# Performance work log

Measured on AMD Instinct MI355X. Metric: run time of the kernel, lower is better.

## Reference

```python
import jax, jax.numpy as jnp
import numpy as np

N = 100000      # nodes
E = 1600000     # edges
G = 1024        # graphs in batch
H = 128         # graph_hidden
F_IN = 38
DEPTH = 4
EPS = 1e-5


def setup_inputs() -> dict:
    key = jax.random.key(0)
    ks = jax.random.split(key, 16)
    inp = {
        "h": jax.random.normal(ks[0], (N, F_IN), jnp.float32),
        "src": jax.random.randint(ks[1], (E,), 0, N, jnp.int32),
        "dst": jax.random.randint(ks[2], (E,), 0, N, jnp.int32),
        "node2graph": jnp.sort(jax.random.randint(ks[3], (N,), 0, G, jnp.int32)),
        "W1": jax.random.normal(ks[4], (F_IN, H), jnp.float32) * 0.1,
        "b1": jnp.zeros((H,), jnp.float32),
        "g1": jnp.ones((H,), jnp.float32),
        "be1": jnp.zeros((H,), jnp.float32),
        "W2s": jax.random.normal(ks[5], (DEPTH - 1, H, H), jnp.float32) * 0.1,
        "b2s": jnp.zeros((DEPTH - 1, H), jnp.float32),
        "g2s": jnp.ones((DEPTH - 1, H), jnp.float32),
        "be2s": jnp.zeros((DEPTH - 1, H), jnp.float32),
        "aw": jax.random.normal(ks[6], (H, 1), jnp.float32) * 0.1,
        "ab": jnp.zeros((1,), jnp.float32),
        "Wf1": jax.random.normal(ks[7], (H, 512), jnp.float32) * 0.1,
        "bf1": jnp.zeros((512,), jnp.float32),
        "gf1": jnp.ones((512,), jnp.float32),
        "bef1": jnp.zeros((512,), jnp.float32),
        "Wl": jax.random.normal(ks[8], (512, 256), jnp.float32) * 0.05,
        "bl": jnp.zeros((256,), jnp.float32),
        "gl": jnp.ones((256,), jnp.float32),
        "bel": jnp.zeros((256,), jnp.float32),
        "Wf2": jax.random.normal(ks[9], (256, 67), jnp.float32) * 0.05,
        "bf2": jnp.zeros((67,), jnp.float32),
    }
    return inp


def _bn(x, g, b):
    # BatchNorm1d in training mode: batch stats (biased variance), eps=1e-5.
    m = jnp.mean(x, axis=0)
    v = jnp.mean(jnp.square(x - m), axis=0)
    return g * (x - m) * jax.lax.rsqrt(v + EPS) + b


def reference(h, src, dst, node2graph,
              W1, b1, g1, be1, W2s, b2s, g2s, be2s,
              aw, ab, Wf1, bf1, gf1, bef1, Wl, bl, gl, bel, Wf2, bf2):
    ones_e = jnp.ones((E,), h.dtype)
    deg_out = jax.ops.segment_sum(ones_e, src, num_segments=N)
    deg_in = jax.ops.segment_sum(ones_e, dst, num_segments=N)
    ns = jax.lax.rsqrt(jnp.maximum(deg_out, 1.0))  # src-side D^{-1/2}
    nd = jax.lax.rsqrt(jnp.maximum(deg_in, 1.0))   # dst-side D^{-1/2}

    def gconv(x, W, b):
        # DGL GraphConv norm='both': D_dst^{-1/2} A D_src^{-1/2} x W + b
        msg = (x * ns[:, None])[src]                      # [E, F] gather
        agg = jax.ops.segment_sum(msg, dst, num_segments=N)
        return (agg * nd[:, None]) @ W + b

    # dropout p = 0.0 -> identity
    x = jax.nn.relu(_bn(gconv(h, W1, b1), g1, be1))
    for i in range(DEPTH - 1):
        x = jax.nn.relu(_bn(gconv(x, W2s[i], b2s[i]), g2s[i], be2s[i]))

    # WeightAndSum readout: sigmoid-gated segment sum over nodes per graph
    atom_weights = x @ aw + ab                            # [N, 1] (pre-sigmoid, returned)
    w = jax.nn.sigmoid(atom_weights)
    hg = jax.ops.segment_sum(x * w, node2graph, num_segments=G)  # [G, H]

    y = jax.nn.relu(_bn(hg @ Wf1 + bf1, gf1, bef1))
    y = jax.nn.relu(_bn(y @ Wl + bl, gl, bel))
    y = jax.nn.sigmoid(y @ Wf2 + bf2)                     # [G, 67]
    return (y, atom_weights)
```

## Files before the change

kernel.cpp:

```cpp
#include <hip/hip_runtime.h>
#include <math.h>

#define NN 100000
#define NE 1600000
#define NG 1024
#define MAXDEG 64
#define EPSB 1e-5f

typedef _Float16 h16;
typedef __attribute__((ext_vector_type(2))) _Float16 h16x2;
typedef __attribute__((ext_vector_type(4))) _Float16 h16x4;
typedef __attribute__((ext_vector_type(8))) _Float16 h16x8;
typedef __attribute__((ext_vector_type(4))) float f32x4;

static __device__ __forceinline__ float sigmoidf_(float x){ return 1.f/(1.f+__expf(-x)); }

__global__ void k_fillall(const int* __restrict__ src, const int* __restrict__ dst,
                          int* __restrict__ degO, int* __restrict__ cnt, int* __restrict__ eidx){
  int e = blockIdx.x*256 + threadIdx.x;
  if (e < NE){
    int s = src[e], d = dst[e];
    atomicAdd(&degO[s], 1);
    int p = atomicAdd(&cnt[d], 1);
    if (p < MAXDEG) eidx[d*MAXDEG + p] = s;
  }
}

__global__ void k_prepg(const int* __restrict__ deg2, const int* __restrict__ n2g,
                        int* __restrict__ eidx, float* __restrict__ ns, float* __restrict__ nd,
                        int* __restrict__ gs, int* __restrict__ ge, float* __restrict__ stats,
                        h16* __restrict__ XA, h16* __restrict__ XB){
  int v = blockIdx.x*256 + threadIdx.x;
  if (v < NN){
    int dO = deg2[v], dI = deg2[NN + v];
    ns[v] = rsqrtf(fmaxf((float)dO, 1.f));
    nd[v] = rsqrtf(fmaxf((float)dI, 1.f));
    int deg = dI > MAXDEG ? MAXDEG : dI;
    int ad = (deg + 7) & ~7;
    if (ad < 8) ad = 8;
    if (ad > MAXDEG) ad = MAXDEG;
    for (int i = deg; i < ad; i++) eidx[v*MAXDEG + i] = NN;
    int g = n2g[v];
    if (v == 0) gs[g] = 0;
    else { int gp = n2g[v-1]; if (gp != g){ gs[g] = v; ge[gp] = v; } }
    if (v == NN-1) ge[g] = NN;
  }
  if (v == NN) ns[NN] = 0.f;
  if (blockIdx.x == 0){
    int t = threadIdx.x;
    for (int j = t; j < 4096; j += 256) stats[j] = 0.f;
    if (t < 128){ XA[(size_t)NN*128 + t] = (h16)0.f; XB[(size_t)NN*128 + t] = (h16)0.f; }
  }
}

__global__ void k_convall(const float* __restrict__ W1, const float* __restrict__ W2s,
                          const float* __restrict__ Wf1, const float* __restrict__ Wl,
                          h16* __restrict__ W1t, h16* __restrict__ W2t,
                          h16* __restrict__ Wf1t, h16* __restrict__ Wlt){
  int i = blockIdx.x*256 + threadIdx.x;
  if (i < 8192){
    int c = i >> 6, k = i & 63;
    W1t[i] = (k < 38) ? (h16)W1[(size_t)k*128 + c] : (h16)0.f;
  } else if (i < 57344){
    int j = i - 8192; int l = j >> 14; int r = j & 16383;
    int c = r >> 7, k = r & 127;
    W2t[j] = (h16)W2s[(size_t)l*16384 + (size_t)k*128 + c];
  } else if (i < 122880){
    int j = i - 57344; int c = j >> 7, k = j & 127;
    Wf1t[j] = (h16)Wf1[(size_t)k*512 + c];
  } else if (i < 253952){
    int j = i - 122880; int c = j >> 9, k = j & 511;
    Wlt[j] = (h16)Wl[(size_t)k*256 + c];
  }
}

__global__ void k_prep1(const float* __restrict__ h, const float* __restrict__ ns,
                        h16* __restrict__ hn){
  int i = blockIdx.x*256 + threadIdx.x;
  if (i >= (NN+1)*40) return;
  int v = i / 40, c = i - v*40;
  float val = (v < NN && c < 38) ? h[(size_t)v*38 + c]*ns[v] : 0.f;
  hn[i] = (h16)val;
}

__global__ __launch_bounds__(256)
void k_gs40(const h16* __restrict__ hn, const int* __restrict__ eidx,
            const int* __restrict__ degI, const float* __restrict__ nd,
            h16* __restrict__ A38){
  int v = (blockIdx.x*256 + threadIdx.x) >> 6;
  int lane = threadIdx.x & 63;
  if (v >= NN) return;
  int deg = degI[v]; if (deg > MAXDEG) deg = MAXDEG;
  int deg8 = (deg + 7) & ~7; if (deg8 < 8) deg8 = 8; if (deg8 > MAXDEG) deg8 = MAXDEG;
  const int* row = eidx + v*MAXDEG;
  int g = lane / 20;
  int c0 = 2*(lane % 20);
  bool act = (lane < 40);
  int gg = g & 1;
  float a0 = 0.f, a1 = 0.f;
  int4 s4 = *(const int4*)(row + 4*gg);
  h16x2 u0={}, u1={}, u2={}, u3={};
  if (act){
    u0 = *(const h16x2*)(hn + (size_t)s4.x*40 + c0);
    u1 = *(const h16x2*)(hn + (size_t)s4.y*40 + c0);
    u2 = *(const h16x2*)(hn + (size_t)s4.z*40 + c0);
    u3 = *(const h16x2*)(hn + (size_t)s4.w*40 + c0);
  }
  for (int e = 0; e < deg8; e += 8){
    int nx = (e + 8 < deg8) ? e + 8 : e;
    int4 s4n = *(const int4*)(row + nx + 4*gg);
    h16x2 n0={}, n1={}, n2={}, n3={};
    if (act){
      n0 = *(const h16x2*)(hn + (size_t)s4n.x*40 + c0);
      n1 = *(const h16x2*)(hn + (size_t)s4n.y*40 + c0);
      n2 = *(const h16x2*)(hn + (size_t)s4n.z*40 + c0);
      n3 = *(const h16x2*)(hn + (size_t)s4n.w*40 + c0);
    }
    a0 += ((float)u0[0] + (float)u1[0]) + ((float)u2[0] + (float)u3[0]);
    a1 += ((float)u0[1] + (float)u1[1]) + ((float)u2[1] + (float)u3[1]);
    u0=n0; u1=n1; u2=n2; u3=n3;
  }
  float b0 = __shfl(a0, lane + 20);
  float b1 = __shfl(a1, lane + 20);
  if (lane < 20){
    float ndv = nd[v];
    h16x2 o; o[0] = (h16)((a0 + b0)*ndv); o[1] = (h16)((a1 + b1)*ndv);
    *(h16x2*)(A38 + (size_t)v*64 + c0) = o;
  } else if (lane < 32){
    h16x2 o; o[0] = (h16)0.f; o[1] = (h16)0.f;
    *(h16x2*)(A38 + (size_t)v*64 + 40 + 2*(lane - 20)) = o;
  }
}

__global__ __launch_bounds__(256)
void k_gs128(const h16* __restrict__ X, const int* __restrict__ eidx,
             const int* __restrict__ degI, const float* __restrict__ ns,
             const float* __restrict__ nd, const float* __restrict__ stats,
             const float* __restrict__ gam, const float* __restrict__ bet,
             h16* __restrict__ agg){
  __shared__ float scs[128], shs[128];
  int t = threadIdx.x;
  if (t < 128){
    float m = stats[t]*(1.f/(float)NN);
    float var = fmaxf(stats[128+t]*(1.f/(float)NN) - m*m, 0.f);
    float inv = rsqrtf(var + EPSB);
    float sc = gam[t]*inv;
    scs[t] = sc; shs[t] = fmaf(-sc, m, bet[t]);
  }
  __syncthreads();
  int v = (blockIdx.x*256 + t) >> 6;
  int lane = t & 63;
  if (v >= NN) return;
  int deg = degI[v]; if (deg > MAXDEG) deg = MAXDEG;
  int deg8 = (deg + 7) & ~7; if (deg8 < 8) deg8 = 8; if (deg8 > MAXDEG) deg8 = MAXDEG;
  const int* row = eidx + v*MAXDEG;
  int half = lane >> 5;
  int c0 = 4*(lane & 31);
  float4 sc = *(const float4*)&scs[c0];
  float4 sh = *(const float4*)&shs[c0];
  float a0=0.f, a1=0.f, a2=0.f, a3=0.f;
  int4 s4 = *(const int4*)(row + 4*half);
  float w0=ns[s4.x], w1=ns[s4.y], w2=ns[s4.z], w3=ns[s4.w];
  h16x4 u0 = *(const h16x4*)(X + (size_t)s4.x*128 + c0);
  h16x4 u1 = *(const h16x4*)(X + (size_t)s4.y*128 + c0);
  h16x4 u2 = *(const h16x4*)(X + (size_t)s4.z*128 + c0);
  h16x4 u3 = *(const h16x4*)(X + (size_t)s4.w*128 + c0);
  for (int e = 0; e < deg8; e += 8){
    int nx = (e + 8 < deg8) ? e + 8 : e;
    int4 s4n = *(const int4*)(row + nx + 4*half);
    float v0=ns[s4n.x], v1=ns[s4n.y], v2=ns[s4n.z], v3=ns[s4n.w];
    h16x4 n0 = *(const h16x4*)(X + (size_t)s4n.x*128 + c0);
    h16x4 n1 = *(const h16x4*)(X + (size_t)s4n.y*128 + c0);
    h16x4 n2 = *(const h16x4*)(X + (size_t)s4n.z*128 + c0);
    h16x4 n3 = *(const h16x4*)(X + (size_t)s4n.w*128 + c0);
    a0 = fmaf(fmaxf(fmaf((float)u0[0], sc.x, sh.x), 0.f), w0, a0);
    a1 = fmaf(fmaxf(fmaf((float)u0[1], sc.y, sh.y), 0.f), w0, a1);
    a2 = fmaf(fmaxf(fmaf((float)u0[2], sc.z, sh.z), 0.f), w0, a2);
    a3 = fmaf(fmaxf(fmaf((float)u0[3], sc.w, sh.w), 0.f), w0, a3);
    a0 = fmaf(fmaxf(fmaf((float)u1[0], sc.x, sh.x), 0.f), w1, a0);
    a1 = fmaf(fmaxf(fmaf((float)u1[1], sc.y, sh.y), 0.f), w1, a1);
    a2 = fmaf(fmaxf(fmaf((float)u1[2], sc.z, sh.z), 0.f), w1, a2);
    a3 = fmaf(fmaxf(fmaf((float)u1[3], sc.w, sh.w), 0.f), w1, a3);
    a0 = fmaf(fmaxf(fmaf((float)u2[0], sc.x, sh.x), 0.f), w2, a0);
    a1 = fmaf(fmaxf(fmaf((float)u2[1], sc.y, sh.y), 0.f), w2, a1);
    a2 = fmaf(fmaxf(fmaf((float)u2[2], sc.z, sh.z), 0.f), w2, a2);
    a3 = fmaf(fmaxf(fmaf((float)u2[3], sc.w, sh.w), 0.f), w2, a3);
    a0 = fmaf(fmaxf(fmaf((float)u3[0], sc.x, sh.x), 0.f), w3, a0);
    a1 = fmaf(fmaxf(fmaf((float)u3[1], sc.y, sh.y), 0.f), w3, a1);
    a2 = fmaf(fmaxf(fmaf((float)u3[2], sc.z, sh.z), 0.f), w3, a2);
    a3 = fmaf(fmaxf(fmaf((float)u3[3], sc.w, sh.w), 0.f), w3, a3);
    u0=n0; u1=n1; u2=n2; u3=n3;
    w0=v0; w1=v1; w2=v2; w3=v3;
  }
  a0 += __shfl_xor(a0, 32);
  a1 += __shfl_xor(a1, 32);
  a2 += __shfl_xor(a2, 32);
  a3 += __shfl_xor(a3, 32);
  if (half == 0){
    float ndv = nd[v];
    h16x4 o;
    o[0] = (h16)(a0*ndv); o[1] = (h16)(a1*ndv);
    o[2] = (h16)(a2*ndv); o[3] = (h16)(a3*ndv);
    *(h16x4*)(agg + (size_t)v*128 + c0) = o;
  }
}

__global__ __launch_bounds__(256)
void k_mgemm(const h16* __restrict__ A, const h16* __restrict__ Wt,
             const float* __restrict__ bias, h16* __restrict__ Cout,
             float* __restrict__ stats, int M, int K, int Nc){
  __shared__ h16 As[128][72];
  __shared__ h16 Bs[128][72];
  __shared__ float sred[2][128];
  int m0 = blockIdx.x*128, n0 = blockIdx.y*128;
  int t = threadIdx.x, w = t>>6, lane = t&63;
  int wr = (w>>1)*64, wc = (w&1)*64;
  f32x4 acc[4][4] = {};

  int ar = t>>3;
  int ac = (t&7)*8;
  for (int k0=0; k0<K; k0+=64){
    #pragma unroll
    for (int rr=0; rr<128; rr+=32){
      int gm = m0 + ar + rr;
      h16x8 val = {};
      if (gm < M) val = *(const h16x8*)(A + (size_t)gm*K + k0 + ac);
      *(h16x8*)&As[ar+rr][ac] = val;
    }
    #pragma unroll
    for (int rr=0; rr<128; rr+=32){
      int gc = n0 + ar + rr;
      h16x8 val = {};
      if (gc < Nc) val = *(const h16x8*)(Wt + (size_t)gc*K + k0 + ac);
      *(h16x8*)&Bs[ar+rr][ac] = val;
    }
    __syncthreads();
    int rsel = lane & 15;
    #pragma unroll
    for (int kk=0; kk<64; kk+=32){
      int ksel = kk + (lane>>4)*8;
      h16x8 af[4], bfr[4];
      #pragma unroll
      for (int i=0;i<4;i++) af[i]  = *(const h16x8*)&As[wr + i*16 + rsel][ksel];
      #pragma unroll
      for (int j=0;j<4;j++) bfr[j] = *(const h16x8*)&Bs[wc + j*16 + rsel][ksel];
      #pragma unroll
      for (int i=0;i<4;i++)
        #pragma unroll
        for (int j=0;j<4;j++)
          acc[i][j] = __builtin_amdgcn_mfma_f32_16x16x32_f16(af[i], bfr[j], acc[i][j], 0, 0, 0);
    }
    __syncthreads();
  }

  float csum[4] = {}, csq[4] = {};
  int colsel = lane & 15, rowsel = (lane>>4)*4;
  #pragma unroll
  for (int j=0;j<4;j++){
    int gc = n0 + wc + j*16 + colsel;
    float bv = (gc < Nc) ? bias[gc] : 0.f;
    #pragma unroll
    for (int i=0;i<4;i++){
      #pragma unroll
      for (int r=0;r<4;r++){
        int gm = m0 + wr + i*16 + rowsel + r;
        if (gm < M && gc < Nc){
          float v = acc[i][j][r] + bv;
          Cout[(size_t)gm*Nc + gc] = (h16)v;
          csum[j] += v; csq[j] += v*v;
        }
      }
    }
  }
  if (stats){
    ((float*)sred)[t] = 0.f;
    __syncthreads();
    #pragma unroll
    for (int j=0;j<4;j++){
      int lc = wc + j*16 + colsel;
      atomicAdd(&sred[0][lc], csum[j]);
      atomicAdd(&sred[1][lc], csq[j]);
    }
    __syncthreads();
    if (t < 128){
      int gc = n0 + t;
      if (gc < Nc){
        atomicAdd(&stats[gc],      sred[0][t]);
        atomicAdd(&stats[Nc + gc], sred[1][t]);
      }
    }
  }
}

__global__ __launch_bounds__(256)
void k_readout(const h16* __restrict__ X, const float* __restrict__ stats,
               const float* __restrict__ gam, const float* __restrict__ bet,
               const float* __restrict__ aw, const float* __restrict__ ab,
               const int* __restrict__ gs, const int* __restrict__ ge,
               float* __restrict__ awout, h16* __restrict__ hg){
  __shared__ float scs[128], shs[128], awv[128];
  __shared__ float red[4][128];
  int t = threadIdx.x;
  if (t < 128){
    float m = stats[t]*(1.f/(float)NN);
    float var = fmaxf(stats[128+t]*(1.f/(float)NN) - m*m, 0.f);
    float inv = rsqrtf(var + EPSB);
    float sc = gam[t]*inv;
    scs[t] = sc; shs[t] = fmaf(-sc, m, bet[t]);
    awv[t] = aw[t];
  }
  __syncthreads();
  int g = blockIdx.x;
  int s = gs[g], e = ge[g];
  int w = t>>6, lane = t&63, c0 = 2*lane;
  float sc0=scs[c0], sc1=scs[c0+1], sh0=shs[c0], sh1=shs[c0+1];
  float aw0=awv[c0], aw1=awv[c0+1];
  float ab0 = ab[0];
  float acc0=0.f, acc1=0.f;
  for (int n = s + w; n < e; n += 4){
    h16x2 u = *(const h16x2*)(X + (size_t)n*128 + c0);
    float x0 = fmaxf(fmaf((float)u[0], sc0, sh0), 0.f);
    float x1 = fmaxf(fmaf((float)u[1], sc1, sh1), 0.f);
    float d = x0*aw0 + x1*aw1;
    #pragma unroll
    for (int o=32;o>0;o>>=1) d += __shfl_xor(d, o);
    float tv = d + ab0;
    if (lane == 0) awout[n] = tv;
    float wn = sigmoidf_(tv);
    acc0 = fmaf(x0, wn, acc0);
    acc1 = fmaf(x1, wn, acc1);
  }
  red[w][c0] = acc0; red[w][c0+1] = acc1;
  __syncthreads();
  if (w == 0){
    float a0 = red[0][c0] + red[1][c0] + red[2][c0] + red[3][c0];
    float a1 = red[0][c0+1] + red[1][c0+1] + red[2][c0+1] + red[3][c0+1];
    h16x2 o; o[0] = (h16)a0; o[1] = (h16)a1;
    *(h16x2*)(hg + (size_t)g*128 + c0) = o;
  }
}

__global__ __launch_bounds__(256)
void k_bnapply_f(const h16* __restrict__ X, h16* __restrict__ Y,
                 const float* __restrict__ stats, const float* __restrict__ gam,
                 const float* __restrict__ bet, float invM, int C, int totalPairs){
  __shared__ float scs[512], shs[512];
  int t = threadIdx.x;
  for (int c = t; c < C; c += 256){
    float m = stats[c]*invM;
    float var = fmaxf(stats[C+c]*invM - m*m, 0.f);
    float inv = rsqrtf(var + EPSB);
    float sc = gam[c]*inv;
    scs[c] = sc; shs[c] = fmaf(-sc, m, bet[c]);
  }
  __syncthreads();
  int i = blockIdx.x*256 + t;
  if (i >= totalPairs) return;
  int pm = (C >> 1) - 1;
  int c0 = 2*(i & pm);
  h16x2 u = *(const h16x2*)(X + 2*(size_t)i);
  float x0 = fmaxf(fmaf((float)u[0], scs[c0],   shs[c0]),   0.f);
  float x1 = fmaxf(fmaf((float)u[1], scs[c0+1], shs[c0+1]), 0.f);
  h16x2 o; o[0] = (h16)x0; o[1] = (h16)x1;
  *(h16x2*)(Y + 2*(size_t)i) = o;
}

__global__ void k_final(const h16* __restrict__ y2, const float* __restrict__ Wf2,
                        const float* __restrict__ bf2v, float* __restrict__ out){
  int idx = blockIdx.x*256 + threadIdx.x;
  if (idx >= NG*67) return;
  int g = idx / 67, c = idx % 67;
  float s = bf2v[c];
  const h16* row = y2 + (size_t)g*256;
  for (int k=0;k<256;k+=2){
    h16x2 u = *(const h16x2*)(row + k);
    s = fmaf((float)u[0], Wf2[(size_t)k*67 + c], s);
    s = fmaf((float)u[1], Wf2[(size_t)(k+1)*67 + c], s);
  }
  out[(size_t)g*67 + c] = sigmoidf_(s);
}

extern "C" void kernel_launch(void* const* d_in, const int* in_sizes, int n_in,
                              void* d_out, int out_size, void* d_ws, size_t ws_size,
                              hipStream_t stream){
  const float* h   = (const float*)d_in[0];
  const int*   src = (const int*)d_in[1];
  const int*   dst = (const int*)d_in[2];
  const int*   n2g = (const int*)d_in[3];
  const float* W1  = (const float*)d_in[4];
  const float* b1  = (const float*)d_in[5];
  const float* g1  = (const float*)d_in[6];
  const float* be1 = (const float*)d_in[7];
  const float* W2s = (const float*)d_in[8];
  const float* b2s = (const float*)d_in[9];
  const float* g2s = (const float*)d_in[10];
  const float* be2s= (const float*)d_in[11];
  const float* aw  = (const float*)d_in[12];
  const float* ab  = (const float*)d_in[13];
  const float* Wf1 = (const float*)d_in[14];
  const float* bf1 = (const float*)d_in[15];
  const float* gf1 = (const float*)d_in[16];
  const float* bef1= (const float*)d_in[17];
  const float* Wl  = (const float*)d_in[18];
  const float* bl  = (const float*)d_in[19];
  const float* gl  = (const float*)d_in[20];
  const float* bel = (const float*)d_in[21];
  const float* Wf2 = (const float*)d_in[22];
  const float* bf2v= (const float*)d_in[23];
  float* out = (float*)d_out;

  char* p = (char*)d_ws;
  auto carve = [&](size_t bytes)->void*{
    void* r = (void*)p; p += (bytes + 255) & ~(size_t)255; return r;
  };
  int* deg2 = (int*)carve((size_t)2*NN*4);
  int* gsge = (int*)carve((size_t)2*NG*4);
  h16* XA   = (h16*)carve((size_t)(NN+1)*128*2);
  h16* XB   = (h16*)carve((size_t)(NN+1)*128*2);
  h16* hn   = (h16*)carve((size_t)(NN+1)*40*2);
  h16* A38  = (h16*)carve((size_t)NN*64*2);
  int* eidx = (int*)carve((size_t)NN*MAXDEG*4);
  float* ns = (float*)carve((size_t)(NN+1)*4);
  float* nd = (float*)carve((size_t)NN*4);
  h16* hg   = (h16*)carve((size_t)NG*128*2);
  h16* y1p  = (h16*)carve((size_t)NG*512*2);
  h16* y1   = (h16*)carve((size_t)NG*512*2);
  h16* y2p  = (h16*)carve((size_t)NG*256*2);
  h16* y2   = (h16*)carve((size_t)NG*256*2);
  float* stats = (float*)carve(4096*4);
  h16* W1t  = (h16*)carve((size_t)128*64*2);
  h16* W2t  = (h16*)carve((size_t)3*128*128*2);
  h16* Wf1t = (h16*)carve((size_t)512*128*2);
  h16* Wlt  = (h16*)carve((size_t)256*512*2);

  int* gs = gsge;
  int* ge = gsge + NG;
  float* st1  = stats;
  float* st2a = stats + 256;
  float* st2b = stats + 512;
  float* st2c = stats + 768;
  float* stf1 = stats + 1024;
  float* stl  = stats + 2048;
  float* st2[3] = { st2a, st2b, st2c };

  hipMemsetAsync(deg2, 0, (size_t)2*NN*4 + (size_t)2*NG*4, stream);

  k_convall<<<(253952+255)/256, 256, 0, stream>>>(W1, W2s, Wf1, Wl, W1t, W2t, Wf1t, Wlt);
  k_fillall<<<(NE+255)/256, 256, 0, stream>>>(src, dst, deg2, deg2 + NN, eidx);
  k_prepg  <<<(NN+1+255)/256, 256, 0, stream>>>(deg2, n2g, eidx, ns, nd, gs, ge, stats, XA, XB);

  const int* degI = deg2 + NN;
  const int nodeBlocks = (NN + 3)/4;
  const int gemmBlocks = (NN + 127)/128;

  k_prep1<<<((NN+1)*40+255)/256, 256, 0, stream>>>(h, ns, hn);
  k_gs40 <<<nodeBlocks, 256, 0, stream>>>(hn, eidx, degI, nd, A38);
  k_mgemm<<<dim3(gemmBlocks,1), 256, 0, stream>>>(A38, W1t, b1, XA, st1, NN, 64, 128);

  const float* stPrev[3] = { st1, st2a, st2b };
  const float* gPrev[3]  = { g1, g2s, g2s + 128 };
  const float* bePrev[3] = { be1, be2s, be2s + 128 };
  for (int i=0;i<3;i++){
    k_gs128<<<nodeBlocks, 256, 0, stream>>>(XA, eidx, degI, ns, nd,
                                            stPrev[i], gPrev[i], bePrev[i], XB);
    k_mgemm<<<dim3(gemmBlocks,1), 256, 0, stream>>>(XB, W2t + (size_t)i*128*128, b2s + i*128,
                                                    XA, st2[i], NN, 128, 128);
  }

  k_readout<<<NG, 256, 0, stream>>>(XA, st2c, g2s + 256, be2s + 256, aw, ab,
                                    gs, ge, out + (size_t)NG*67, hg);

  k_mgemm<<<dim3(NG/128, 4), 256, 0, stream>>>(hg, Wf1t, bf1, y1p, stf1, NG, 128, 512);
  k_bnapply_f<<<(NG*256+255)/256, 256, 0, stream>>>(y1p, y1, stf1, gf1, bef1,
                                                    1.0f/(float)NG, 512, NG*256);
  k_mgemm<<<dim3(NG/128, 2), 256, 0, stream>>>(y1, Wlt, bl, y2p, stl, NG, 512, 256);
  k_bnapply_f<<<(NG*128+255)/256, 256, 0, stream>>>(y2p, y2, stl, gl, bel,
                                                    1.0f/(float)NG, 256, NG*128);
  k_final<<<(NG*67+255)/256, 256, 0, stream>>>(y2, Wf2, bf2v, out);
}
```

Baseline: 725.1 us.

## Replace global-atomic adjacency build with bucketed counting sort via shared-memory histograms

Degree counting and neighbour-list filling no longer use per-edge global atomics. Edges are now bucketed by dst/64 and src/64 with a per-block shared-memory histogram, a three-pass prefix scan and a scatter. Per-bucket blocks then build eidx, the degrees and the normalisers using shared-memory atomics. The aim is to cut contention and scattered global atomic traffic, at the cost of six extra launches and an extra 12.8MB sorted buffer pass. The graph start/end computation also now fills empty graphs, which replaces the memset.

```diff
diff --git a/kernel.cpp b/kernel.cpp
--- a/kernel.cpp
+++ b/kernel.cpp
@@ -7,6 +7,12 @@
 #define MAXDEG 64
 #define EPSB 1e-5f
 
+#define NBUK 1563
+#define NBLK 256
+#define EPB  6250
+#define FLAT (2*NBUK*NBLK)
+#define NCH  ((FLAT + 1023)/1024)
+
 typedef _Float16 h16;
 typedef __attribute__((ext_vector_type(2))) _Float16 h16x2;
 typedef __attribute__((ext_vector_type(4))) _Float16 h16x4;
@@ -15,35 +21,148 @@
 
 static __device__ __forceinline__ float sigmoidf_(float x){ return 1.f/(1.f+__expf(-x)); }
 
-__global__ void k_fillall(const int* __restrict__ src, const int* __restrict__ dst,
-                          int* __restrict__ degO, int* __restrict__ cnt, int* __restrict__ eidx){
-  int e = blockIdx.x*256 + threadIdx.x;
-  if (e < NE){
-    int s = src[e], d = dst[e];
-    atomicAdd(&degO[s], 1);
-    int p = atomicAdd(&cnt[d], 1);
-    if (p < MAXDEG) eidx[d*MAXDEG + p] = s;
-  }
-}
-
-__global__ void k_prepg(const int* __restrict__ deg2, const int* __restrict__ n2g,
-                        int* __restrict__ eidx, float* __restrict__ ns, float* __restrict__ nd,
+__global__ __launch_bounds__(256)
+void k_hist(const int* __restrict__ src, const int* __restrict__ dst,
+            int* __restrict__ blockHist){
+  __shared__ int hd[NBUK];
+  __shared__ int hs[NBUK];
+  int b = blockIdx.x, t = threadIdx.x;
+  for (int j = t; j < NBUK; j += 256){ hd[j] = 0; hs[j] = 0; }
+  __syncthreads();
+  int e0 = b*EPB, e1 = e0 + EPB;
+  for (int i = e0 + t; i < e1; i += 256){
+    atomicAdd(&hd[dst[i]>>6], 1);
+    atomicAdd(&hs[src[i]>>6], 1);
+  }
+  __syncthreads();
+  for (int j = t; j < NBUK; j += 256){
+    blockHist[(size_t)j*NBLK + b] = hd[j];
+    blockHist[(size_t)(NBUK + j)*NBLK + b] = hs[j];
+  }
+}
+
+__global__ __launch_bounds__(256)
+void k_scan1(int* __restrict__ data, int* __restrict__ csum){
+  __shared__ int s[256];
+  int blk = blockIdx.x, t = threadIdx.x;
+  int base = blk*1024 + t*4;
+  int v0=0,v1=0,v2=0,v3=0;
+  if (base+0 < FLAT) v0 = data[base+0];
+  if (base+1 < FLAT) v1 = data[base+1];
+  if (base+2 < FLAT) v2 = data[base+2];
+  if (base+3 < FLAT) v3 = data[base+3];
+  int tot = v0+v1+v2+v3;
+  s[t] = tot; __syncthreads();
+  for (int o=1;o<256;o<<=1){ int x = (t>=o)? s[t-o]:0; __syncthreads(); s[t]+=x; __syncthreads(); }
+  int excl = s[t] - tot;
+  if (t == 255) csum[blk] = s[255];
+  if (base+0 < FLAT) data[base+0] = excl;
+  if (base+1 < FLAT) data[base+1] = excl + v0;
+  if (base+2 < FLAT) data[base+2] = excl + v0 + v1;
+  if (base+3 < FLAT) data[base+3] = excl + v0 + v1 + v2;
+}
+
+__global__ void k_scan2(int* __restrict__ csum){
+  __shared__ int s[1024];
+  int t = threadIdx.x;
+  int x = (t < NCH) ? csum[t] : 0;
+  s[t] = x; __syncthreads();
+  for (int o=1;o<1024;o<<=1){ int y = (t>=o)? s[t-o]:0; __syncthreads(); s[t]+=y; __syncthreads(); }
+  if (t < NCH) csum[t] = s[t] - x;
+}
+
+__global__ __launch_bounds__(256)
+void k_scan3(int* __restrict__ data, const int* __restrict__ csum){
+  int blk = blockIdx.x, t = threadIdx.x;
+  int add = csum[blk];
+  int base = blk*1024 + t*4;
+  if (base+0 < FLAT) data[base+0] += add;
+  if (base+1 < FLAT) data[base+1] += add;
+  if (base+2 < FLAT) data[base+2] += add;
+  if (base+3 < FLAT) data[base+3] += add;
+}
+
+__global__ __launch_bounds__(256)
+void k_scatter(const int* __restrict__ src, const int* __restrict__ dst,
+               const int* __restrict__ scanned, unsigned int* __restrict__ sortedBuf){
+  __shared__ int bd[NBUK];
+  __shared__ int bs[NBUK];
+  int b = blockIdx.x, t = threadIdx.x;
+  for (int j = t; j < NBUK; j += 256){
+    bd[j] = scanned[(size_t)j*NBLK + b];
+    bs[j] = scanned[(size_t)(NBUK + j)*NBLK + b];
+  }
+  __syncthreads();
+  int e0 = b*EPB, e1 = e0 + EPB;
+  for (int i = e0 + t; i < e1; i += 256){
+    int s = src[i], d = dst[i];
+    int posD = atomicAdd(&bd[d>>6], 1);
+    sortedBuf[posD] = (unsigned int)s | ((unsigned int)(d & 63) << 20);
+    int posS = atomicAdd(&bs[s>>6], 1);
+    sortedBuf[posS] = (unsigned int)s;
+  }
+}
+
+__global__ __launch_bounds__(256)
+void k_build(const unsigned int* __restrict__ sortedBuf, const int* __restrict__ scanned,
+             int* __restrict__ eidx, int* __restrict__ degI,
+             float* __restrict__ ns, float* __restrict__ nd){
+  __shared__ int cnt[64];
+  int k = blockIdx.x, t = threadIdx.x;
+  int v0 = k*64;
+  int nv = NN - v0; if (nv > 64) nv = 64;
+  if (t < 64) cnt[t] = 0;
+  __syncthreads();
+  int startD = scanned[(size_t)k*NBLK];
+  int endD   = scanned[(size_t)(k+1)*NBLK];
+  for (int i = startD + t; i < endD; i += 256){
+    unsigned int u = sortedBuf[i];
+    int lid = (int)(u >> 20);
+    int slot = atomicAdd(&cnt[lid], 1);
+    if (slot < MAXDEG) eidx[(size_t)(v0 + lid)*MAXDEG + slot] = (int)(u & 0xFFFFFu);
+  }
+  __syncthreads();
+  if (t < nv){
+    int v = v0 + t;
+    int dI = cnt[t];
+    degI[v] = dI;
+    nd[v] = rsqrtf(fmaxf((float)dI, 1.f));
+    int c = dI > MAXDEG ? MAXDEG : dI;
+    int ad = (c + 7) & ~7; if (ad < 8) ad = 8; if (ad > MAXDEG) ad = MAXDEG;
+    for (int i = c; i < ad; i++) eidx[(size_t)v*MAXDEG + i] = NN;
+  }
+  __syncthreads();
+  if (t < 64) cnt[t] = 0;
+  __syncthreads();
+  int startS = scanned[(size_t)(NBUK + k)*NBLK];
+  int endS   = (k+1 < NBUK) ? scanned[(size_t)(NBUK + k + 1)*NBLK] : 2*NE;
+  for (int i = startS + t; i < endS; i += 256){
+    atomicAdd(&cnt[sortedBuf[i] & 63u], 1);
+  }
+  __syncthreads();
+  if (t < nv) ns[v0 + t] = rsqrtf(fmaxf((float)cnt[t], 1.f));
+}
+
+__global__ void k_prepg(const int* __restrict__ n2g,
                         int* __restrict__ gs, int* __restrict__ ge, float* __restrict__ stats,
-                        h16* __restrict__ XA, h16* __restrict__ XB){
+                        float* __restrict__ ns, h16* __restrict__ XA, h16* __restrict__ XB){
   int v = blockIdx.x*256 + threadIdx.x;
   if (v < NN){
-    int dO = deg2[v], dI = deg2[NN + v];
-    ns[v] = rsqrtf(fmaxf((float)dO, 1.f));
-    nd[v] = rsqrtf(fmaxf((float)dI, 1.f));
-    int deg = dI > MAXDEG ? MAXDEG : dI;
-    int ad = (deg + 7) & ~7;
-    if (ad < 8) ad = 8;
-    if (ad > MAXDEG) ad = MAXDEG;
-    for (int i = deg; i < ad; i++) eidx[v*MAXDEG + i] = NN;
     int g = n2g[v];
-    if (v == 0) gs[g] = 0;
-    else { int gp = n2g[v-1]; if (gp != g){ gs[g] = v; ge[gp] = v; } }
-    if (v == NN-1) ge[g] = NN;
+    if (v == 0){
+      for (int q = 0; q <= g; q++) gs[q] = 0;
+      for (int q = 0; q < g; q++) ge[q] = 0;
+    } else {
+      int gp = n2g[v-1];
+      if (gp != g){
+        for (int q = gp+1; q <= g; q++) gs[q] = v;
+        for (int q = gp; q < g; q++) ge[q] = v;
+      }
+    }
+    if (v == NN-1){
+      for (int q = g+1; q < NG; q++) gs[q] = NN;
+      for (int q = g; q < NG; q++) ge[q] = NN;
+    }
   }
   if (v == NN) ns[NN] = 0.f;
   if (blockIdx.x == 0){
@@ -413,15 +532,18 @@
   auto carve = [&](size_t bytes)->void*{
     void* r = (void*)p; p += (bytes + 255) & ~(size_t)255; return r;
   };
-  int* deg2 = (int*)carve((size_t)2*NN*4);
-  int* gsge = (int*)carve((size_t)2*NG*4);
   h16* XA   = (h16*)carve((size_t)(NN+1)*128*2);
   h16* XB   = (h16*)carve((size_t)(NN+1)*128*2);
   h16* hn   = (h16*)carve((size_t)(NN+1)*40*2);
   h16* A38  = (h16*)carve((size_t)NN*64*2);
   int* eidx = (int*)carve((size_t)NN*MAXDEG*4);
+  unsigned int* sortedBuf = (unsigned int*)carve((size_t)2*NE*4);
+  int* blockHist = (int*)carve((size_t)FLAT*4);
+  int* csum = (int*)carve(1024*4);
+  int* degI = (int*)carve((size_t)NN*4);
   float* ns = (float*)carve((size_t)(NN+1)*4);
   float* nd = (float*)carve((size_t)NN*4);
+  int* gsge = (int*)carve((size_t)2*NG*4);
   h16* hg   = (h16*)carve((size_t)NG*128*2);
   h16* y1p  = (h16*)carve((size_t)NG*512*2);
   h16* y1   = (h16*)carve((size_t)NG*512*2);
@@ -443,13 +565,16 @@
   float* stl  = stats + 2048;
   float* st2[3] = { st2a, st2b, st2c };
 
-  hipMemsetAsync(deg2, 0, (size_t)2*NN*4 + (size_t)2*NG*4, stream);
-
   k_convall<<<(253952+255)/256, 256, 0, stream>>>(W1, W2s, Wf1, Wl, W1t, W2t, Wf1t, Wlt);
-  k_fillall<<<(NE+255)/256, 256, 0, stream>>>(src, dst, deg2, deg2 + NN, eidx);
-  k_prepg  <<<(NN+1+255)/256, 256, 0, stream>>>(deg2, n2g, eidx, ns, nd, gs, ge, stats, XA, XB);
-
-  const int* degI = deg2 + NN;
+  k_prepg  <<<(NN+1+255)/256, 256, 0, stream>>>(n2g, gs, ge, stats, ns, XA, XB);
+
+  k_hist   <<<NBLK, 256, 0, stream>>>(src, dst, blockHist);
+  k_scan1  <<<NCH, 256, 0, stream>>>(blockHist, csum);
+  k_scan2  <<<1, 1024, 0, stream>>>(csum);
+  k_scan3  <<<NCH, 256, 0, stream>>>(blockHist, csum);
+  k_scatter<<<NBLK, 256, 0, stream>>>(src, dst, blockHist, sortedBuf);
+  k_build  <<<NBUK, 256, 0, stream>>>(sortedBuf, blockHist, eidx, degI, ns, nd);
+
   const int nodeBlocks = (NN + 3)/4;
   const int gemmBlocks = (NN + 127)/128;
 
```

Result: faster. 654.0 us (-9.8%).
